# Kernel optimization log

Hardware: AMD Instinct MI355X
Metric: run time of the kernel (lower is better)

## Reference

```python
import jax, jax.numpy as jnp
import numpy as np

B, M, N = 32, 2048, 2048
W_PRIMAL, W_DUAL, W_STAT, W_COMP = 0.1, 0.1, 0.6, 0.2


def setup_inputs() -> dict:
    key = jax.random.key(0)
    k1, k2, k3, k4, k5 = jax.random.split(key, 5)
    return {
        "x_hat": jax.random.normal(k1, (B * N,), dtype=jnp.float32),
        "lam_hat": jax.random.normal(k2, (B * M,), dtype=jnp.float32),
        "A": jax.random.normal(k3, (B, M, N), dtype=jnp.float32),
        "b_pad": jax.random.normal(k4, (B, M), dtype=jnp.float32),
        "c_pad": jax.random.normal(k5, (B, N), dtype=jnp.float32),
        "b_mask": jnp.ones((B, M), dtype=bool),
        "c_mask": jnp.ones((B, N), dtype=bool),
    }


def reference(x_hat, lam_hat, A, b_pad, c_pad, b_mask, c_mask):
    # Uniform sizes: x_hat is the concatenation of B vectors of length N,
    # lam_hat of B vectors of length M. b_mask/c_mask are unused by the
    # original forward (full padding assumed here).
    b, m, n = A.shape
    x = x_hat.reshape(b, n)
    lam = lam_hat.reshape(b, m)

    # Batched mat-vec products (the spmm calls in the original, fp32 math).
    Ax_minus_b = jnp.einsum("bmn,bn->bm", A, x) - b_pad        # [B, M]
    At_lambda = jnp.einsum("bmn,bm->bn", A, lam)               # [B, N]

    # Per-sample mean, summed over batch, then * (1/B) == global mean
    # (sizes are uniform).
    loss_primal = jnp.mean(jnp.square(jax.nn.relu(Ax_minus_b)))
    loss_dual = jnp.mean(jnp.square(jax.nn.relu(-lam)))
    loss_stat = jnp.mean(jnp.square(At_lambda + c_pad))
    loss_comp = jnp.mean(jnp.square(lam * Ax_minus_b))

    total = (W_PRIMAL * loss_primal + W_DUAL * loss_dual
             + W_STAT * loss_stat + W_COMP * loss_comp)
    return total
```

## Files before the change

### kernel.cpp

```cpp
#include <hip/hip_runtime.h>

#define BB 32
#define MM 2048
#define NN 2048
#define ROWS 64
#define CHUNKS (MM / ROWS)
#define THREADS 256

typedef float f32x4 __attribute__((ext_vector_type(4)));

#define P0 ((size_t)BB * CHUNKS * NN)
#define P1 (P0 + 2 * BB * CHUNKS)
#define FIN_BLOCKS 256

__device__ __forceinline__ float waveReduceSum(float v) {
#pragma unroll
    for (int off = 32; off > 0; off >>= 1)
        v += __shfl_down(v, off, 64);
    return v;
}

template <int CTRL>
__device__ __forceinline__ float dppAdd(float v) {
    int s = __builtin_amdgcn_update_dpp(0, __builtin_bit_cast(int, v),
                                        CTRL, 0xF, 0xF, false);
    return v + __builtin_bit_cast(float, s);
}

__device__ __forceinline__ float group16Reduce(float v) {
    v = dppAdd<0x111>(v);
    v = dppAdd<0x112>(v);
    v = dppAdd<0x114>(v);
    v = dppAdd<0x118>(v);
    return v;
}

__global__ __launch_bounds__(THREADS, 4) void fused_main(
    const float* __restrict__ x_hat, const float* __restrict__ lam_hat,
    const float* __restrict__ A, const float* __restrict__ b_pad,
    float* __restrict__ ws) {
    const int b = blockIdx.y;
    const int chunk = blockIdx.x;
    const int m0 = chunk * ROWS;
    const int t = threadIdx.x;

    __shared__ float lamS[ROWS];
    __shared__ __align__(16) float wp[ROWS * 16];

    if (t < ROWS) lamS[t] = lam_hat[b * MM + m0 + t];
    __syncthreads();

    const f32x4* xv = (const f32x4*)(x_hat + (size_t)b * NN);
    const f32x4 x0 = xv[t];
    const f32x4 x1 = xv[256 + t];

    f32x4 at0 = (f32x4)(0.f);
    f32x4 at1 = (f32x4)(0.f);

    const f32x4* Ab = (const f32x4*)(A + ((size_t)b * MM + (size_t)m0) * NN);

    f32x4 a0 = __builtin_nontemporal_load(Ab + t);
    f32x4 a1 = __builtin_nontemporal_load(Ab + 256 + t);

#define ROW_BODY(r)                                              \
    do {                                                         \
        const float lm = lamS[r];                                \
        f32x4 d = a0 * x0 + a1 * x1;                             \
        at0 += a0 * lm;                                          \
        at1 += a1 * lm;                                          \
        float dot = (d.x + d.y) + (d.z + d.w);                   \
        dot = group16Reduce(dot);                                \
        if ((t & 15) == 15) wp[(r) * 16 + (t >> 4)] = dot;       \
    } while (0)

    for (int r = 0; r < ROWS - 1; ++r) {
        const f32x4* np = Ab + (size_t)(r + 1) * (NN / 4);
        f32x4 n0 = __builtin_nontemporal_load(np + t);
        f32x4 n1 = __builtin_nontemporal_load(np + 256 + t);

        ROW_BODY(r);

        a0 = n0;
        a1 = n1;
    }
    ROW_BODY(ROWS - 1);
#undef ROW_BODY
    __syncthreads();

    if (t < 64) {
        const f32x4* wpv = (const f32x4*)wp;
        f32x4 s4 = wpv[t * 4 + 0] + wpv[t * 4 + 1] +
                   wpv[t * 4 + 2] + wpv[t * 4 + 3];
        float y = (s4.x + s4.y) + (s4.z + s4.w) - b_pad[b * MM + m0 + t];
        float lm = lamS[t];
        float ry = fmaxf(y, 0.f);
        float pr = ry * ry;
        float c = lm * y;
        float cm = c * c;
        pr = waveReduceSum(pr);
        cm = waveReduceSum(cm);
        if (t == 0) {
            float* prcm = ws + P0 + ((size_t)b * CHUNKS + chunk) * 2;
            prcm[0] = pr;
            prcm[1] = cm;
        }
    }

    f32x4* dst = (f32x4*)(ws + ((size_t)b * CHUNKS + chunk) * NN);
    dst[t] = at0;
    dst[256 + t] = at1;
}

__global__ __launch_bounds__(256) void finalize_partial(
    const float* __restrict__ ws_ro, const float* __restrict__ c_pad,
    const float* __restrict__ lam_hat, float* __restrict__ ws) {
    const int t = threadIdx.x;
    const int b = blockIdx.x >> 3;
    const int g = blockIdx.x & 7;
    const int c = t & 63;
    const int kq = t >> 6;

    const f32x4* base = (const f32x4*)ws_ro +
        ((size_t)b * CHUNKS + (size_t)kq * 8) * (NN / 4) + (size_t)g * 64 + c;
    f32x4 s = (f32x4)(0.f);
#pragma unroll
    for (int k = 0; k < 8; ++k) s += base[(size_t)k * (NN / 4)];

    __shared__ __align__(16) f32x4 part[4][64];
    part[kq][c] = s;
    __syncthreads();

    float stat = 0.f, dual = 0.f;
    if (t < 64) {
        f32x4 v = part[0][c] + part[1][c] + part[2][c] + part[3][c];
        f32x4 cp = ((const f32x4*)c_pad)[(size_t)b * (NN / 4) + (size_t)g * 64 + c];
        v += cp;
        stat = v.x * v.x + v.y * v.y + v.z * v.z + v.w * v.w;

        f32x4 l = ((const f32x4*)lam_hat)[(size_t)blockIdx.x * 64 + c];
        float r0 = fmaxf(-l.x, 0.f), r1 = fmaxf(-l.y, 0.f);
        float r2 = fmaxf(-l.z, 0.f), r3 = fmaxf(-l.w, 0.f);
        dual = r0 * r0 + r1 * r1 + r2 * r2 + r3 * r3;

        stat = waveReduceSum(stat);
        dual = waveReduceSum(dual);
        if (t == 0) {
            ws[P1 + (size_t)blockIdx.x * 2 + 0] = stat;
            ws[P1 + (size_t)blockIdx.x * 2 + 1] = dual;
        }
    }
}

__global__ __launch_bounds__(256) void combine_kernel(
    const float* __restrict__ ws_ro, float* __restrict__ out) {
    const int t = threadIdx.x;
    const int wave = t >> 6;
    const int lane = t & 63;
    float v = 0.f;
    if (wave == 0) {
#pragma unroll
        for (int j = 0; j < 4; ++j)
            v += ws_ro[P1 + (size_t)((lane << 2) | j) * 2 + 0];
    } else if (wave == 1) {
#pragma unroll
        for (int j = 0; j < 4; ++j)
            v += ws_ro[P1 + (size_t)((lane << 2) | j) * 2 + 1];
    } else if (wave == 2) {
#pragma unroll
        for (int j = 0; j < 16; ++j)
            v += ws_ro[P0 + (size_t)((lane << 4) | j) * 2 + 0];
    } else {
#pragma unroll
        for (int j = 0; j < 16; ++j)
            v += ws_ro[P0 + (size_t)((lane << 4) | j) * 2 + 1];
    }
    v = waveReduceSum(v);
    __shared__ float s[4];
    if (lane == 0) s[wave] = v;
    __syncthreads();
    if (t == 0) {
        const float invBM = 1.0f / (float)(BB * MM);
        const float invBN = 1.0f / (float)(BB * NN);
        float stat = s[0] * invBN;
        float dual = s[1] * invBM;
        float primal = s[2] * invBM;
        float comp = s[3] * invBM;
        out[0] = 0.1f * primal + 0.1f * dual + 0.6f * stat + 0.2f * comp;
    }
}

extern "C" void kernel_launch(void* const* d_in, const int* in_sizes, int n_in,
                              void* d_out, int out_size, void* d_ws, size_t ws_size,
                              hipStream_t stream) {
    const float* x_hat   = (const float*)d_in[0];
    const float* lam_hat = (const float*)d_in[1];
    const float* A       = (const float*)d_in[2];
    const float* b_pad   = (const float*)d_in[3];
    const float* c_pad   = (const float*)d_in[4];
    float* out = (float*)d_out;
    float* ws = (float*)d_ws;

    dim3 grid(CHUNKS, BB);
    fused_main<<<grid, THREADS, 0, stream>>>(x_hat, lam_hat, A, b_pad, ws);

    finalize_partial<<<FIN_BLOCKS, 256, 0, stream>>>(ws, c_pad, lam_hat, ws);

    combine_kernel<<<1, 256, 0, stream>>>(ws, out);
}
```

Measured before the change: 665.4 us.

## Assign rows per wave with LDS-staged x and swizzled block order

Work in the main kernel is split so each wavefront owns 16 full rows of A, instead of the whole block sharing each row. x is staged in LDS, and the per-row dot product becomes a full-wave shuffle reduction instead of 16-lane DPP groups plus a cross-group LDS pass. Per-wave A^T·lambda accumulators are merged through LDS with serialized barriers. Block indices are swizzled to change the order in which memory is visited. Nontemporal loads are dropped, and register pressure rises with 16 live vector loads per thread.

```diff
diff --git a/kernel.cpp b/kernel.cpp
--- a/kernel.cpp
+++ b/kernel.cpp
@@ -20,78 +20,101 @@
     return v;
 }
 
-template <int CTRL>
-__device__ __forceinline__ float dppAdd(float v) {
-    int s = __builtin_amdgcn_update_dpp(0, __builtin_bit_cast(int, v),
-                                        CTRL, 0xF, 0xF, false);
-    return v + __builtin_bit_cast(float, s);
-}
-
-__device__ __forceinline__ float group16Reduce(float v) {
-    v = dppAdd<0x111>(v);
-    v = dppAdd<0x112>(v);
-    v = dppAdd<0x114>(v);
-    v = dppAdd<0x118>(v);
-    return v;
-}
-
 __global__ __launch_bounds__(THREADS, 4) void fused_main(
     const float* __restrict__ x_hat, const float* __restrict__ lam_hat,
     const float* __restrict__ A, const float* __restrict__ b_pad,
     float* __restrict__ ws) {
-    const int b = blockIdx.y;
-    const int chunk = blockIdx.x;
+    const int lin = blockIdx.y * CHUNKS + blockIdx.x;
+    const int swz = (lin & 7) * 128 + (lin >> 3);
+    const int b = swz >> 5;
+    const int chunk = swz & 31;
     const int m0 = chunk * ROWS;
     const int t = threadIdx.x;
-
+    const int w = t >> 6;
+    const int l = t & 63;
+
+    __shared__ __align__(16) f32x4 xS[512];
+    __shared__ __align__(16) f32x4 atS[512];
     __shared__ float lamS[ROWS];
-    __shared__ __align__(16) float wp[ROWS * 16];
-
+    __shared__ float wp[ROWS];
+
+    const f32x4* xv = (const f32x4*)(x_hat + (size_t)b * NN);
+    xS[t] = xv[t];
+    xS[256 + t] = xv[256 + t];
     if (t < ROWS) lamS[t] = lam_hat[b * MM + m0 + t];
     __syncthreads();
 
-    const f32x4* xv = (const f32x4*)(x_hat + (size_t)b * NN);
-    const f32x4 x0 = xv[t];
-    const f32x4 x1 = xv[256 + t];
-
-    f32x4 at0 = (f32x4)(0.f);
-    f32x4 at1 = (f32x4)(0.f);
-
-    const f32x4* Ab = (const f32x4*)(A + ((size_t)b * MM + (size_t)m0) * NN);
-
-    f32x4 a0 = __builtin_nontemporal_load(Ab + t);
-    f32x4 a1 = __builtin_nontemporal_load(Ab + 256 + t);
-
-#define ROW_BODY(r)                                              \
-    do {                                                         \
-        const float lm = lamS[r];                                \
-        f32x4 d = a0 * x0 + a1 * x1;                             \
-        at0 += a0 * lm;                                          \
-        at1 += a1 * lm;                                          \
-        float dot = (d.x + d.y) + (d.z + d.w);                   \
-        dot = group16Reduce(dot);                                \
-        if ((t & 15) == 15) wp[(r) * 16 + (t >> 4)] = dot;       \
-    } while (0)
-
-    for (int r = 0; r < ROWS - 1; ++r) {
-        const f32x4* np = Ab + (size_t)(r + 1) * (NN / 4);
-        f32x4 n0 = __builtin_nontemporal_load(np + t);
-        f32x4 n1 = __builtin_nontemporal_load(np + 256 + t);
-
-        ROW_BODY(r);
-
-        a0 = n0;
-        a1 = n1;
-    }
-    ROW_BODY(ROWS - 1);
-#undef ROW_BODY
-    __syncthreads();
+    const int RV = NN / 4;
+    const f32x4* Aw = (const f32x4*)(A + ((size_t)b * MM + (size_t)(m0 + 16 * w)) * NN);
+
+    f32x4 at0 = (f32x4)(0.f), at1 = (f32x4)(0.f), at2 = (f32x4)(0.f),
+          at3 = (f32x4)(0.f), at4 = (f32x4)(0.f), at5 = (f32x4)(0.f),
+          at6 = (f32x4)(0.f), at7 = (f32x4)(0.f);
+
+    f32x4 c0, c1, c2, c3, c4, c5, c6, c7;
+    f32x4 n0, n1, n2, n3, n4, n5, n6, n7;
+
+#define LOAD8(p, v)                                                       \
+    do {                                                                  \
+        v##0 = (p)[l];       v##1 = (p)[l + 64];  v##2 = (p)[l + 128];    \
+        v##3 = (p)[l + 192]; v##4 = (p)[l + 256]; v##5 = (p)[l + 320];    \
+        v##6 = (p)[l + 384]; v##7 = (p)[l + 448];                         \
+    } while (0)
+
+#define BODY(v, RL)                                                       \
+    do {                                                                  \
+        const float lm = lamS[16 * w + (RL)];                             \
+        f32x4 d = v##0 * xS[l];                                           \
+        d += v##1 * xS[l + 64];  d += v##2 * xS[l + 128];                 \
+        d += v##3 * xS[l + 192]; d += v##4 * xS[l + 256];                 \
+        d += v##5 * xS[l + 320]; d += v##6 * xS[l + 384];                 \
+        d += v##7 * xS[l + 448];                                          \
+        at0 += v##0 * lm; at1 += v##1 * lm; at2 += v##2 * lm;             \
+        at3 += v##3 * lm; at4 += v##4 * lm; at5 += v##5 * lm;             \
+        at6 += v##6 * lm; at7 += v##7 * lm;                               \
+        float dot = (d.x + d.y) + (d.z + d.w);                            \
+        dot = waveReduceSum(dot);                                         \
+        if (l == 0) wp[16 * w + (RL)] = dot;                              \
+    } while (0)
+
+#define ROT8()                                                            \
+    do {                                                                  \
+        c0 = n0; c1 = n1; c2 = n2; c3 = n3;                               \
+        c4 = n4; c5 = n5; c6 = n6; c7 = n7;                               \
+    } while (0)
+
+    LOAD8(Aw, c);
+    for (int rl = 0; rl < 15; ++rl) {
+        const f32x4* np = Aw + (size_t)(rl + 1) * RV;
+        LOAD8(np, n);
+        BODY(c, rl);
+        ROT8();
+    }
+    BODY(c, 15);
+#undef LOAD8
+#undef BODY
+#undef ROT8
+    __syncthreads();
+
+#define ATSTORE(op)                                                       \
+    do {                                                                  \
+        atS[l]       op at0; atS[l + 64]  op at1;                         \
+        atS[l + 128] op at2; atS[l + 192] op at3;                         \
+        atS[l + 256] op at4; atS[l + 320] op at5;                         \
+        atS[l + 384] op at6; atS[l + 448] op at7;                         \
+    } while (0)
+    if (w == 0) ATSTORE(=);
+    __syncthreads();
+    if (w == 1) ATSTORE(+=);
+    __syncthreads();
+    if (w == 2) ATSTORE(+=);
+    __syncthreads();
+    if (w == 3) ATSTORE(+=);
+    __syncthreads();
+#undef ATSTORE
 
     if (t < 64) {
-        const f32x4* wpv = (const f32x4*)wp;
-        f32x4 s4 = wpv[t * 4 + 0] + wpv[t * 4 + 1] +
-                   wpv[t * 4 + 2] + wpv[t * 4 + 3];
-        float y = (s4.x + s4.y) + (s4.z + s4.w) - b_pad[b * MM + m0 + t];
+        float y = wp[t] - b_pad[b * MM + m0 + t];
         float lm = lamS[t];
         float ry = fmaxf(y, 0.f);
         float pr = ry * ry;
@@ -107,8 +130,8 @@
     }
 
     f32x4* dst = (f32x4*)(ws + ((size_t)b * CHUNKS + chunk) * NN);
-    dst[t] = at0;
-    dst[256 + t] = at1;
+    dst[t] = atS[t];
+    dst[256 + t] = atS[256 + t];
 }
 
 __global__ __launch_bounds__(256) void finalize_partial(
@@ -137,9 +160,9 @@
         v += cp;
         stat = v.x * v.x + v.y * v.y + v.z * v.z + v.w * v.w;
 
-        f32x4 l = ((const f32x4*)lam_hat)[(size_t)blockIdx.x * 64 + c];
-        float r0 = fmaxf(-l.x, 0.f), r1 = fmaxf(-l.y, 0.f);
-        float r2 = fmaxf(-l.z, 0.f), r3 = fmaxf(-l.w, 0.f);
+        f32x4 lv = ((const f32x4*)lam_hat)[(size_t)blockIdx.x * 64 + c];
+        float r0 = fmaxf(-lv.x, 0.f), r1 = fmaxf(-lv.y, 0.f);
+        float r2 = fmaxf(-lv.z, 0.f), r3 = fmaxf(-lv.w, 0.f);
         dual = r0 * r0 + r1 * r1 + r2 * r2 + r3 * r3;
 
         stat = waveReduceSum(stat);
```

Result: slower. 914.1 us (+37.4%).
